# Performance work log

Hardware: AMD Instinct MI355X
Metric: run time of the kernel (lower is better)

Reference implementation:

```python
import jax, jax.numpy as jnp
import numpy as np

MAX_NUM_BINS = 200
BIN_SIZE = 500
NUM_NEIGHBORS = 5
DIST_MULT = 0.1


def setup_inputs() -> dict:
    key = jax.random.key(0)
    k1, k2 = jax.random.split(key)
    points = jax.random.normal(k1, (2, 5000, 128), dtype=jnp.float32)
    rotations = jax.random.normal(k2, (128, MAX_NUM_BINS // 2), dtype=jnp.float32)
    return {"points": points, "rotations": rotations}


def reference(points, rotations):
    # points: [B, N, D], rotations: [D, max_num_bins//2]
    B, N, D = points.shape
    nbins = N // BIN_SIZE  # module requires N % BIN_SIZE == 0

    # LSH bin assignment: project onto nbins//2 random directions, sign-split into nbins bins
    mul = jnp.einsum('bnd,dh->bnh', points, rotations[:, :nbins // 2])  # [B,N,nbins//2]
    cmul = jnp.concatenate([mul, -mul], axis=-1)                        # [B,N,nbins]
    bin_idx = jnp.argmax(cmul, axis=-1)                                 # [B,N]
    # equal-size bins via argsort of bin id (matches tf argsort+reshape)
    bins_split = jnp.argsort(bin_idx, axis=-1).reshape(B, nbins, BIN_SIZE)  # [B,nbins,S]

    # gather points per bin
    parts = jnp.take_along_axis(points, bins_split.reshape(B, N, 1), axis=1)
    parts = parts.reshape(B, nbins, BIN_SIZE, D)

    # per-bin pairwise distance -> gaussian kernel
    na = jnp.sum(parts * parts, axis=-1)                                # [B,nbins,S]
    gram = jnp.einsum('bcid,bcjd->bcij', parts, parts)                  # [B,nbins,S,S]
    dist = jnp.sqrt(jnp.maximum(na[..., :, None] - 2.0 * gram + na[..., None, :], 1e-6))
    dm = jnp.exp(-DIST_MULT * dist)                                     # [B,nbins,S,S]

    # top-k neighbors within each bin
    vals, idx = jax.lax.top_k(dm, NUM_NEIGHBORS)                        # [B,nbins,S,K]

    # map local bin indices back to global point indices
    bs_flat = bins_split.reshape(B * nbins, BIN_SIZE)
    dst = jnp.take_along_axis(bs_flat, idx.reshape(B * nbins, BIN_SIZE * NUM_NEIGHBORS), axis=1)
    dst = dst.reshape(B, nbins, BIN_SIZE, NUM_NEIGHBORS)
    src = jnp.broadcast_to(bins_split[..., None], dst.shape)
    bidx = jnp.broadcast_to(jnp.arange(B)[:, None, None, None], dst.shape)

    # scatter-add into dense [B,N,N] (sparse.add sums duplicate entries)
    out = jnp.zeros((B, N, N), dtype=points.dtype)
    out = out.at[bidx.reshape(-1), src.reshape(-1), dst.reshape(-1)].add(vals.reshape(-1))
    return out
```

## Files before the change

### kernel.cpp

```cpp
#include <hip/hip_runtime.h>
#include <cfloat>
#include <math.h>

#define NPTS   5000
#define BATCH  2
#define DIM    128
#define NBINS  10
#define BINSZ  500
#define TOPK   5
#define ROTCOLS 100

#define KB_PTS 64
#define KB_STR 129
__global__ void k_bins(const float* __restrict__ pts, const float* __restrict__ rot,
                       int* __restrict__ bin_idx, double* __restrict__ na) {
    __shared__ float P[KB_PTS * KB_STR];
    __shared__ float rotL[DIM * 5];
    int tid = threadIdx.x;
    for (int f = tid; f < DIM * 5; f += 256)
        rotL[f] = rot[(f / 5) * ROTCOLS + (f % 5)];

    int p0  = blockIdx.x * KB_PTS;
    int npb = min(KB_PTS, BATCH * NPTS - p0);

    for (int f = tid; f < npb * DIM; f += 256) {
        int r = f >> 7, d = f & 127;
        P[r * KB_STR + d] = pts[(size_t)(p0 + r) * DIM + d];
    }
    __syncthreads();

    int p = tid >> 2;
    int s = tid & 3;
    double acc[5] = {0., 0., 0., 0., 0.};
    double sq = 0.;
    const float* row = &P[p * KB_STR + s * 32];
    for (int j = 0; j < 32; ++j) {
        double v = (double)row[j];
        sq += v * v;
        int d = s * 32 + j;
#pragma unroll
        for (int h = 0; h < 5; ++h) acc[h] += v * (double)rotL[d * 5 + h];
    }
#pragma unroll
    for (int m = 1; m < 4; m <<= 1) {
#pragma unroll
        for (int h = 0; h < 5; ++h) acc[h] += __shfl_xor(acc[h], m, 4);
        sq += __shfl_xor(sq, m, 4);
    }
    if (s == 0 && p < npb) {
        double best = acc[0]; int bc = 0;
#pragma unroll
        for (int c = 1; c < NBINS; ++c) {
            double v = (c < 5) ? acc[c] : -acc[c - 5];
            if (v > best) { best = v; bc = c; }
        }
        bin_idx[p0 + p] = bc;
        na[p0 + p] = sq;
    }
}

__global__ void k_sort(const int* __restrict__ bin_idx, int* __restrict__ order) {
    const int b = blockIdx.x;
    const int t = threadIdx.x;
    const int NPT = (NPTS + 255) / 256;
    int start = t * NPT;
    int end   = min(NPTS, start + NPT);

    int cnt[NBINS];
#pragma unroll
    for (int c = 0; c < NBINS; ++c) cnt[c] = 0;
    for (int i = start; i < end; ++i) {
        int c = bin_idx[b * NPTS + i];
#pragma unroll
        for (int k = 0; k < NBINS; ++k) cnt[k] += (c == k);
    }

    __shared__ int hist[NBINS * 256];
#pragma unroll
    for (int c = 0; c < NBINS; ++c) hist[c * 256 + t] = cnt[c];
    __syncthreads();

    int base = t * NBINS;
    int s = 0;
#pragma unroll
    for (int k = 0; k < NBINS; ++k) s += hist[base + k];
    __shared__ int scan[256];
    scan[t] = s;
    __syncthreads();
    for (int off = 1; off < 256; off <<= 1) {
        int v = (t >= off) ? scan[t - off] : 0;
        __syncthreads();
        scan[t] += v;
        __syncthreads();
    }
    int run = scan[t] - s;
#pragma unroll
    for (int k = 0; k < NBINS; ++k) { int h = hist[base + k]; hist[base + k] = run; run += h; }
    __syncthreads();

    int ofs[NBINS];
#pragma unroll
    for (int c = 0; c < NBINS; ++c) ofs[c] = hist[c * 256 + t];
    for (int i = start; i < end; ++i) {
        int c = bin_idx[b * NPTS + i];
        int pos = 0;
#pragma unroll
        for (int k = 0; k < NBINS; ++k) {
            if (c == k) pos = ofs[k];
            ofs[k] += (c == k);
        }
        order[b * NPTS + pos] = i;
    }
}

#define RT    16
#define NRT   32
#define CTILE 64
#define RSTRD 130
#define CSTR  132
#define NCT   8
#define ROWQ  (NPTS/4)

__launch_bounds__(256, 3)
__global__ void k_chunks(const float* __restrict__ pts, const double* __restrict__ na,
                         const int* __restrict__ order, float* __restrict__ out) {
    __shared__ double rowPd[RT * RSTRD];
    __shared__ float  colP[CTILE * CSTR];
    __shared__ double naC[CTILE];
    __shared__ double naRs[RT];
    __shared__ int    ordR[RT];

    int blk   = blockIdx.x;
    int rt    = blk & (NRT - 1);
    int chunk = blk >> 5;
    int b     = chunk / NBINS;
    int c     = chunk % NBINS;
    int tid   = threadIdx.x;
    int row0  = rt * RT;
    int rowCount = min(RT, BINSZ - row0);

    const int*   ordBase = order + b * NPTS + c * BINSZ;
    const float* ptsB    = pts + (size_t)b * NPTS * DIM;

    for (int f = tid; f < rowCount * (DIM / 4); f += 256) {
        int r = f >> 5;
        int q = f & 31;
        int g = ordBase[row0 + r];
        float4 v = *(const float4*)(ptsB + (size_t)g * DIM + q * 4);
        double2 d01; d01.x = (double)v.x; d01.y = (double)v.y;
        double2 d23; d23.x = (double)v.z; d23.y = (double)v.w;
        *(double2*)(&rowPd[r * RSTRD + q * 4 + 0]) = d01;
        *(double2*)(&rowPd[r * RSTRD + q * 4 + 2]) = d23;
    }
    if (tid < rowCount) {
        int g = ordBase[row0 + tid];
        ordR[tid] = g;
        naRs[tid] = na[b * NPTS + g];
    }
    __syncthreads();

    int rg = tid >> 5;
    int cg = tid & 31;

    double naRr0 = (rg     < rowCount) ? naRs[rg]     : 0.;
    double naRr1 = (rg + 8 < rowCount) ? naRs[rg + 8] : 0.;

    double tv[2][TOPK];
    int    tl[2][TOPK];
#pragma unroll
    for (int ii = 0; ii < 2; ++ii)
#pragma unroll
        for (int k = 0; k < TOPK; ++k) { tv[ii][k] = DBL_MAX; tl[ii][k] = 0x7fffffff; }

    const int totalZ = rowCount * ROWQ;

    for (int ct = 0; ct < NCT; ++ct) {
        int col0 = ct * CTILE;
        int colCount = min(CTILE, BINSZ - col0);
        __syncthreads();
        for (int f = tid; f < colCount * (DIM / 4); f += 256) {
            int j = f >> 5;
            int q = f & 31;
            int g = ordBase[col0 + j];
            float4 v = *(const float4*)(ptsB + (size_t)g * DIM + q * 4);
            *(float4*)(&colP[j * CSTR + q * 4]) = v;
        }
        if (tid < colCount) {
            int g = ordBase[col0 + tid];
            naC[tid] = na[b * NPTS + g];
        }
        __syncthreads();

        {
            float4 z = make_float4(0.f, 0.f, 0.f, 0.f);
            int z0 = (ct * totalZ) / NCT, z1 = ((ct + 1) * totalZ) / NCT;
            for (int f = z0 + tid; f < z1; f += 256) {
                int r = f / ROWQ;
                int q = f - r * ROWQ;
                float* outRow = out + ((size_t)b * NPTS + ordR[r]) * NPTS;
                *(float4*)(outRow + 4 * q) = z;
            }
        }

        double acc00 = 0., acc01 = 0., acc10 = 0., acc11 = 0.;

        for (int q = 0; q < DIM / 4; ++q) {
            double2 a0lo = *(const double2*)(&rowPd[rg * RSTRD + q * 4 + 0]);
            double2 a0hi = *(const double2*)(&rowPd[rg * RSTRD + q * 4 + 2]);
            double2 a1lo = *(const double2*)(&rowPd[(rg + 8) * RSTRD + q * 4 + 0]);
            double2 a1hi = *(const double2*)(&rowPd[(rg + 8) * RSTRD + q * 4 + 2]);
            float4 b0 = *(const float4*)(&colP[cg * CSTR + q * 4]);
            float4 b1 = *(const float4*)(&colP[(cg + 32) * CSTR + q * 4]);
            double b00 = (double)b0.x, b01 = (double)b0.y,
                   b02 = (double)b0.z, b03 = (double)b0.w;
            double b10 = (double)b1.x, b11 = (double)b1.y,
                   b12 = (double)b1.z, b13 = (double)b1.w;
            acc00 += a0lo.x * b00 + a0lo.y * b01 + a0hi.x * b02 + a0hi.y * b03;
            acc01 += a0lo.x * b10 + a0lo.y * b11 + a0hi.x * b12 + a0hi.y * b13;
            acc10 += a1lo.x * b00 + a1lo.y * b01 + a1hi.x * b02 + a1hi.y * b03;
            acc11 += a1lo.x * b10 + a1lo.y * b11 + a1hi.x * b12 + a1hi.y * b13;
        }

#pragma unroll
        for (int jj = 0; jj < 2; ++jj) {
            int j = cg + 32 * jj;
            if (j < colCount) {
                int    cl = col0 + j;
                double nc = naC[j];
                double a0 = (jj == 0) ? acc00 : acc01;
                double a1 = (jj == 0) ? acc10 : acc11;
                double cv0 = fmax(naRr0 + nc - 2. * a0, 1e-6);
                double cv1 = fmax(naRr1 + nc - 2. * a1, 1e-6);
                int cl0 = cl, cl1 = cl;
#pragma unroll
                for (int k = 0; k < TOPK; ++k) {
                    bool lt0 = (cv0 < tv[0][k]);
                    double ov0 = tv[0][k]; int ol0 = tl[0][k];
                    if (lt0) { tv[0][k] = cv0; tl[0][k] = cl0; cv0 = ov0; cl0 = ol0; }
                    bool lt1 = (cv1 < tv[1][k]);
                    double ov1 = tv[1][k]; int ol1 = tl[1][k];
                    if (lt1) { tv[1][k] = cv1; tl[1][k] = cl1; cv1 = ov1; cl1 = ol1; }
                }
            }
        }
    }

#pragma unroll
    for (int m = 1; m < 32; m <<= 1) {
#pragma unroll
        for (int ii = 0; ii < 2; ++ii) {
            double rv[TOPK]; int rl[TOPK];
#pragma unroll
            for (int k = 0; k < TOPK; ++k) {
                rv[k] = __shfl_xor(tv[ii][k], m, 32);
                rl[k] = __shfl_xor(tl[ii][k], m, 32);
            }
#pragma unroll
            for (int k = 0; k < TOPK; ++k) {
                double cv = rv[k]; int cl = rl[k];
#pragma unroll
                for (int s = 0; s < TOPK; ++s) {
                    bool better = (cv < tv[ii][s]) || (cv == tv[ii][s] && cl < tl[ii][s]);
                    double ov = tv[ii][s]; int ol = tl[ii][s];
                    if (better) { tv[ii][s] = cv; tl[ii][s] = cl; cv = ov; cl = ol; }
                }
            }
        }
    }

    __syncthreads();

    if (cg == 0) {
#pragma unroll
        for (int ii = 0; ii < 2; ++ii) {
            int r = rg + 8 * ii;
            if (r < rowCount) {
                int src = ordR[r];
                float* outRow = out + ((size_t)b * NPTS + src) * NPTS;
#pragma unroll
                for (int k = 0; k < TOPK; ++k) {
                    double dist = sqrt(tv[ii][k]);
                    double dm   = exp(-0.1 * dist);
                    int dst = ordBase[tl[ii][k]];
                    outRow[dst] = (float)dm;
                }
            }
        }
    }
}

extern "C" void kernel_launch(void* const* d_in, const int* in_sizes, int n_in,
                              void* d_out, int out_size, void* d_ws, size_t ws_size,
                              hipStream_t stream) {
    const float* pts = (const float*)d_in[0];
    const float* rot = (const float*)d_in[1];
    float* out = (float*)d_out;

    double* na      = (double*)d_ws;
    int*    bin_idx = (int*)((char*)d_ws + 80000);
    int*    order   = (int*)((char*)d_ws + 120000);

    k_bins<<<(BATCH * NPTS + KB_PTS - 1) / KB_PTS, 256, 0, stream>>>(pts, rot, bin_idx, na);
    k_sort<<<BATCH, 256, 0, stream>>>(bin_idx, order);
    k_chunks<<<BATCH * NBINS * NRT, 256, 0, stream>>>(pts, na, order, out);
}
```

Before: 295.5 us.

## Shrink k_chunks tiles and split the dot-product K dimension across half-warps

Measured after the change: 292.3 us. About the same (-1.1%).

```diff
diff --git a/kernel.cpp b/kernel.cpp
--- a/kernel.cpp
+++ b/kernel.cpp
@@ -113,15 +113,15 @@
     }
 }
 
-#define RT    16
-#define NRT   32
-#define CTILE 64
+#define RT    8
+#define NRT   63
+#define CTILE 32
 #define RSTRD 130
 #define CSTR  132
-#define NCT   8
+#define NCT   16
 #define ROWQ  (NPTS/4)
 
-__launch_bounds__(256, 3)
+__launch_bounds__(256, 6)
 __global__ void k_chunks(const float* __restrict__ pts, const double* __restrict__ na,
                          const int* __restrict__ order, float* __restrict__ out) {
     __shared__ double rowPd[RT * RSTRD];
@@ -131,8 +131,8 @@
     __shared__ int    ordR[RT];
 
     int blk   = blockIdx.x;
-    int rt    = blk & (NRT - 1);
-    int chunk = blk >> 5;
+    int rt    = blk % NRT;
+    int chunk = blk / NRT;
     int b     = chunk / NBINS;
     int c     = chunk % NBINS;
     int tid   = threadIdx.x;
@@ -159,34 +159,34 @@
     }
     __syncthreads();
 
-    int rg = tid >> 5;
-    int cg = tid & 31;
-
-    double naRr0 = (rg     < rowCount) ? naRs[rg]     : 0.;
-    double naRr1 = (rg + 8 < rowCount) ? naRs[rg + 8] : 0.;
-
-    double tv[2][TOPK];
-    int    tl[2][TOPK];
-#pragma unroll
-    for (int ii = 0; ii < 2; ++ii)
-#pragma unroll
-        for (int k = 0; k < TOPK; ++k) { tv[ii][k] = DBL_MAX; tl[ii][k] = 0x7fffffff; }
+    int cg  = tid & 15;
+    int ks  = (tid >> 4) & 1;
+    int rg  = tid >> 5;
+    int cgm = tid & 31;
+    const int q0 = ks * 64;
+
+    double naRr = (rg < rowCount) ? naRs[rg] : 0.;
+
+    double tv[TOPK];
+    int    tl[TOPK];
+#pragma unroll
+    for (int k = 0; k < TOPK; ++k) { tv[k] = DBL_MAX; tl[k] = 0x7fffffff; }
 
     const int totalZ = rowCount * ROWQ;
 
     for (int ct = 0; ct < NCT; ++ct) {
-        int col0 = ct * CTILE;
-        int colCount = min(CTILE, BINSZ - col0);
+        int col0T = ct * CTILE;
+        int colCount = min(CTILE, BINSZ - col0T);
         __syncthreads();
         for (int f = tid; f < colCount * (DIM / 4); f += 256) {
             int j = f >> 5;
             int q = f & 31;
-            int g = ordBase[col0 + j];
+            int g = ordBase[col0T + j];
             float4 v = *(const float4*)(ptsB + (size_t)g * DIM + q * 4);
             *(float4*)(&colP[j * CSTR + q * 4]) = v;
         }
         if (tid < colCount) {
-            int g = ordBase[col0 + tid];
+            int g = ordBase[col0T + tid];
             naC[tid] = na[b * NPTS + g];
         }
         __syncthreads();
@@ -202,89 +202,67 @@
             }
         }
 
-        double acc00 = 0., acc01 = 0., acc10 = 0., acc11 = 0.;
-
-        for (int q = 0; q < DIM / 4; ++q) {
-            double2 a0lo = *(const double2*)(&rowPd[rg * RSTRD + q * 4 + 0]);
-            double2 a0hi = *(const double2*)(&rowPd[rg * RSTRD + q * 4 + 2]);
-            double2 a1lo = *(const double2*)(&rowPd[(rg + 8) * RSTRD + q * 4 + 0]);
-            double2 a1hi = *(const double2*)(&rowPd[(rg + 8) * RSTRD + q * 4 + 2]);
-            float4 b0 = *(const float4*)(&colP[cg * CSTR + q * 4]);
-            float4 b1 = *(const float4*)(&colP[(cg + 32) * CSTR + q * 4]);
-            double b00 = (double)b0.x, b01 = (double)b0.y,
-                   b02 = (double)b0.z, b03 = (double)b0.w;
-            double b10 = (double)b1.x, b11 = (double)b1.y,
-                   b12 = (double)b1.z, b13 = (double)b1.w;
-            acc00 += a0lo.x * b00 + a0lo.y * b01 + a0hi.x * b02 + a0hi.y * b03;
-            acc01 += a0lo.x * b10 + a0lo.y * b11 + a0hi.x * b12 + a0hi.y * b13;
-            acc10 += a1lo.x * b00 + a1lo.y * b01 + a1hi.x * b02 + a1hi.y * b03;
-            acc11 += a1lo.x * b10 + a1lo.y * b11 + a1hi.x * b12 + a1hi.y * b13;
-        }
-
-#pragma unroll
-        for (int jj = 0; jj < 2; ++jj) {
-            int j = cg + 32 * jj;
-            if (j < colCount) {
-                int    cl = col0 + j;
-                double nc = naC[j];
-                double a0 = (jj == 0) ? acc00 : acc01;
-                double a1 = (jj == 0) ? acc10 : acc11;
-                double cv0 = fmax(naRr0 + nc - 2. * a0, 1e-6);
-                double cv1 = fmax(naRr1 + nc - 2. * a1, 1e-6);
-                int cl0 = cl, cl1 = cl;
-#pragma unroll
-                for (int k = 0; k < TOPK; ++k) {
-                    bool lt0 = (cv0 < tv[0][k]);
-                    double ov0 = tv[0][k]; int ol0 = tl[0][k];
-                    if (lt0) { tv[0][k] = cv0; tl[0][k] = cl0; cv0 = ov0; cl0 = ol0; }
-                    bool lt1 = (cv1 < tv[1][k]);
-                    double ov1 = tv[1][k]; int ol1 = tl[1][k];
-                    if (lt1) { tv[1][k] = cv1; tl[1][k] = cl1; cv1 = ov1; cl1 = ol1; }
-                }
+        double acc0 = 0., acc1 = 0.;
+        for (int q = 0; q < 64; q += 4) {
+            const int qq = q0 + q;
+            double2 alo = *(const double2*)(&rowPd[rg * RSTRD + qq + 0]);
+            double2 ahi = *(const double2*)(&rowPd[rg * RSTRD + qq + 2]);
+            float4 f0 = *(const float4*)(&colP[cg * CSTR + qq]);
+            float4 f1 = *(const float4*)(&colP[(cg + 16) * CSTR + qq]);
+            double b0x = (double)f0.x, b0y = (double)f0.y, b0z = (double)f0.z, b0w = (double)f0.w;
+            double b1x = (double)f1.x, b1y = (double)f1.y, b1z = (double)f1.z, b1w = (double)f1.w;
+            acc0 += alo.x * b0x + alo.y * b0y + ahi.x * b0z + ahi.y * b0w;
+            acc1 += alo.x * b1x + alo.y * b1y + ahi.x * b1z + ahi.y * b1w;
+        }
+
+        acc0 += __shfl_xor(acc0, 16, 64);
+        acc1 += __shfl_xor(acc1, 16, 64);
+
+        double sel = ks ? acc1 : acc0;
+        int    col = cg + (ks ? 16 : 0);
+        if (col < colCount) {
+            int    ci = col0T + col;
+            double cv = fmax(naRr + naC[col] - 2. * sel, 1e-6);
+#pragma unroll
+            for (int k = 0; k < TOPK; ++k) {
+                bool lt = (cv < tv[k]);
+                double ov = tv[k]; int ol = tl[k];
+                if (lt) { tv[k] = cv; tl[k] = ci; cv = ov; ci = ol; }
             }
         }
     }
 
 #pragma unroll
     for (int m = 1; m < 32; m <<= 1) {
-#pragma unroll
-        for (int ii = 0; ii < 2; ++ii) {
-            double rv[TOPK]; int rl[TOPK];
-#pragma unroll
-            for (int k = 0; k < TOPK; ++k) {
-                rv[k] = __shfl_xor(tv[ii][k], m, 32);
-                rl[k] = __shfl_xor(tl[ii][k], m, 32);
+        double rv[TOPK]; int rl[TOPK];
+#pragma unroll
+        for (int k = 0; k < TOPK; ++k) {
+            rv[k] = __shfl_xor(tv[k], m, 32);
+            rl[k] = __shfl_xor(tl[k], m, 32);
+        }
+#pragma unroll
+        for (int k = 0; k < TOPK; ++k) {
+            double cv = rv[k]; int cl = rl[k];
+#pragma unroll
+            for (int s = 0; s < TOPK; ++s) {
+                bool better = (cv < tv[s]) || (cv == tv[s] && cl < tl[s]);
+                double ov = tv[s]; int ol = tl[s];
+                if (better) { tv[s] = cv; tl[s] = cl; cv = ov; cl = ol; }
             }
-#pragma unroll
-            for (int k = 0; k < TOPK; ++k) {
-                double cv = rv[k]; int cl = rl[k];
-#pragma unroll
-                for (int s = 0; s < TOPK; ++s) {
-                    bool better = (cv < tv[ii][s]) || (cv == tv[ii][s] && cl < tl[ii][s]);
-                    double ov = tv[ii][s]; int ol = tl[ii][s];
-                    if (better) { tv[ii][s] = cv; tl[ii][s] = cl; cv = ov; cl = ol; }
-                }
-            }
-        }
-    }
-
-    __syncthreads();
-
-    if (cg == 0) {
-#pragma unroll
-        for (int ii = 0; ii < 2; ++ii) {
-            int r = rg + 8 * ii;
-            if (r < rowCount) {
-                int src = ordR[r];
-                float* outRow = out + ((size_t)b * NPTS + src) * NPTS;
-#pragma unroll
-                for (int k = 0; k < TOPK; ++k) {
-                    double dist = sqrt(tv[ii][k]);
-                    double dm   = exp(-0.1 * dist);
-                    int dst = ordBase[tl[ii][k]];
-                    outRow[dst] = (float)dm;
-                }
-            }
+        }
+    }
+
+    __syncthreads();
+
+    if (cgm == 0 && rg < rowCount) {
+        int src = ordR[rg];
+        float* outRow = out + ((size_t)b * NPTS + src) * NPTS;
+#pragma unroll
+        for (int k = 0; k < TOPK; ++k) {
+            double dist = sqrt(tv[k]);
+            double dm   = exp(-0.1 * dist);
+            int dst = ordBase[tl[k]];
+            outRow[dst] = (float)dm;
         }
     }
 }
```
